# Optimization experiments

Measured on AMD Instinct MI355X. Metric: run time of the kernel, lower is better.

## Reference

```python
import jax, jax.numpy as jnp
import numpy as np

B, S, E = 2, 2048, 2048
H = 16              # num value heads
D = E // H // 2     # = 64, half head dim (Q/K head dim)
LAMBDA_INIT = 0.8 - 0.6 * float(np.exp(-0.3 * 12))
NORM_EPS = 1e-5


def setup_inputs() -> dict:
    key = jax.random.key(0)
    ks = jax.random.split(key, 10)
    std = 0.02
    x = jax.random.normal(ks[0], (B, S, E), jnp.float32)
    Wq = jax.random.normal(ks[1], (E, E), jnp.float32) * std
    Wk = jax.random.normal(ks[2], (E, E), jnp.float32) * std
    Wv = jax.random.normal(ks[3], (E, E), jnp.float32) * std
    Wo = jax.random.normal(ks[4], (E, E), jnp.float32) * std
    lambda_q1 = jax.random.normal(ks[5], (D,), jnp.float32) * 0.1
    lambda_q2 = jax.random.normal(ks[6], (D,), jnp.float32) * 0.1
    lambda_k1 = jax.random.normal(ks[7], (D,), jnp.float32) * 0.1
    lambda_k2 = jax.random.normal(ks[8], (D,), jnp.float32) * 0.1
    norm_w = jnp.ones((2 * D,), jnp.float32)
    # standard RoPE angle table: (S, D//2)
    inv_freq = 1.0 / (10000.0 ** (np.arange(0, D, 2, dtype=np.float32) / D))
    ang = np.outer(np.arange(S, dtype=np.float32), inv_freq)
    freqs_cos = jnp.asarray(np.cos(ang), jnp.float32)
    freqs_sin = jnp.asarray(np.sin(ang), jnp.float32)
    return {"x": x, "Wq": Wq, "Wk": Wk, "Wv": Wv, "Wo": Wo,
            "lambda_q1": lambda_q1, "lambda_q2": lambda_q2,
            "lambda_k1": lambda_k1, "lambda_k2": lambda_k2,
            "norm_w": norm_w, "freqs_cos": freqs_cos, "freqs_sin": freqs_sin,
            "start_pos": 0}


def _rope(t, cos, sin):
    # t: (B, S, nh, D); complex rotation over pairs along last dim
    tr = t.reshape(*t.shape[:-1], -1, 2)
    tre, tim = tr[..., 0], tr[..., 1]
    c = cos[None, :, None, :]
    s = sin[None, :, None, :]
    out_re = tre * c - tim * s
    out_im = tre * s + tim * c
    return jnp.stack([out_re, out_im], axis=-1).reshape(t.shape)


def reference(x, Wq, Wk, Wv, Wo, lambda_q1, lambda_q2, lambda_k1, lambda_k2,
              norm_w, freqs_cos, freqs_sin, start_pos):
    bsz, tgt_len, _ = x.shape
    scaling = D ** (-0.5)
    q = (x @ Wq.T).reshape(bsz, tgt_len, 2 * H, D)
    k = (x @ Wk.T).reshape(bsz, tgt_len, 2 * H, D)
    v = (x @ Wv.T).reshape(bsz, tgt_len, H, 2 * D)
    q = _rope(q, freqs_cos, freqs_sin)
    k = _rope(k, freqs_cos, freqs_sin)
    q = (q * scaling).transpose(0, 2, 1, 3)      # (B, 2H, S, D)
    keys = k.transpose(0, 2, 1, 3)               # (B, 2H, S, D)
    values = v.transpose(0, 2, 1, 3)             # (B, H, S, 2D)
    scores = jnp.einsum('bhsd,bhtd->bhst', q, keys)
    causal = jnp.where(jnp.arange(tgt_len)[None, :] > jnp.arange(tgt_len)[:, None],
                       jnp.float32(-jnp.inf), jnp.float32(0.0))
    scores = scores + causal
    attn = jax.nn.softmax(scores.astype(jnp.float32), axis=-1)
    lam1 = jnp.exp(jnp.sum(lambda_q1 * lambda_k1))
    lam2 = jnp.exp(jnp.sum(lambda_q2 * lambda_k2))
    lambda_full = lam1 - lam2 + LAMBDA_INIT
    attn = attn.reshape(bsz, H, 2, tgt_len, tgt_len)
    attn_diff = attn[:, :, 0] - lambda_full * attn[:, :, 1]   # (B, H, S, S)
    ctx = jnp.einsum('bhst,bhtd->bhsd', attn_diff, values)    # (B, H, S, 2D)
    # per-head RMSNorm over 2D channel dim
    ctx = ctx * jax.lax.rsqrt(jnp.mean(ctx * ctx, axis=-1, keepdims=True) + NORM_EPS)
    ctx = ctx * norm_w
    ctx = ctx.transpose(0, 2, 1, 3).reshape(bsz, tgt_len, H * 2 * D)
    return ctx @ Wo.T
```

## Files before the change

### kernel.cpp

```cpp
#include <hip/hip_runtime.h>
#include <hip/hip_bf16.h>
#include <stdint.h>

typedef __hip_bfloat16 bf16;
typedef __attribute__((ext_vector_type(8))) short short8;
typedef __attribute__((ext_vector_type(4))) short s4v;
typedef __attribute__((ext_vector_type(4))) float floatx4;

#define MFMA16(a, b, c) __builtin_amdgcn_mfma_f32_16x16x32_bf16((a), (b), (c), 0, 0, 0)
#define LAMBDA_INIT_F 0.7836057665f

__device__ __forceinline__ void async16(const void* g, void* l) {
    __builtin_amdgcn_global_load_lds(
        (const __attribute__((address_space(1))) void*)g,
        (__attribute__((address_space(3))) void*)(uintptr_t)l,
        16, 0, 0);
}

__device__ __forceinline__ float loadf(const void* p, size_t idx, int isbf) {
    if (isbf) return __bfloat162float(((const bf16*)p)[idx]);
    return ((const float*)p)[idx];
}

__global__ void detect_dtype(const unsigned short* __restrict__ x, int* __restrict__ flag) {
    const int t = threadIdx.x;
    const unsigned short u = x[2 * t];
    const int e = (u >> 7) & 0xFF;
    int sane = (e >= 110 && e <= 130) ? 1 : 0;
#pragma unroll
    for (int m = 32; m > 0; m >>= 1) sane += __shfl_xor(sane, m);
    if (t == 0) flag[0] = (sane >= 32) ? 1 : 0;
}

__global__ __launch_bounds__(256) void to_bf16(const void* __restrict__ src,
                                               bf16* __restrict__ dst, int n,
                                               const int* __restrict__ flag,
                                               int skip_if_bf16) {
    if (skip_if_bf16 && flag[0]) return;
    const int i = (blockIdx.x * 256 + threadIdx.x) * 8;
    if (i >= n) return;
    if (flag[0]) {
        *(short8*)(dst + i) = *(const short8*)((const bf16*)src + i);
    } else {
        const float* f = (const float*)src + i;
        short8 r;
#pragma unroll
        for (int j = 0; j < 8; ++j) {
            bf16 h = __float2bfloat16(f[j]);
            r[j] = __builtin_bit_cast(short, h);
        }
        *(short8*)(dst + i) = r;
    }
}

__device__ __forceinline__ void gemm_core(const bf16* __restrict__ A,
                                          const bf16* __restrict__ B,
                                          void* __restrict__ C,
                                          int N, int K, int bm, int bn,
                                          const int* __restrict__ flag,
                                          const void* __restrict__ fcos,
                                          const void* __restrict__ fsin,
                                          int mode, bf16* As, bf16* Bs) {
    const int tid  = threadIdx.x;
    const int lane = tid & 63;
    const int quad = lane >> 4;
    const int l16  = lane & 15;
    const int w    = tid >> 6;
    const int wr   = w >> 1, wc = w & 1;

    floatx4 acc[4][4];
#pragma unroll
    for (int i = 0; i < 4; ++i)
#pragma unroll
        for (int j = 0; j < 4; ++j)
#pragma unroll
            for (int r = 0; r < 4; ++r) acc[i][j][r] = 0.0f;

    for (int k0 = 0; k0 < K; k0 += 32) {
        __syncthreads();
#pragma unroll
        for (int i = 0; i < 2; ++i) {
            const int c     = i * 256 + tid;
            const int row   = c >> 2;
            const int inner = c & 3;
            async16(A + (size_t)(bm * 128 + row) * K + k0 + inner * 8, (char*)As + c * 16);
            async16(B + (size_t)(bn * 128 + row) * K + k0 + inner * 8, (char*)Bs + c * 16);
        }
        __syncthreads();

        short8 af[4], bfr[4];
#pragma unroll
        for (int i = 0; i < 4; ++i)
            af[i] = *(const short8*)((const char*)As + (wr * 64 + i * 16 + l16) * 64 + quad * 16);
#pragma unroll
        for (int j = 0; j < 4; ++j)
            bfr[j] = *(const short8*)((const char*)Bs + (wc * 64 + j * 16 + l16) * 64 + quad * 16);
#pragma unroll
        for (int i = 0; i < 4; ++i)
#pragma unroll
            for (int j = 0; j < 4; ++j)
                acc[i][j] = MFMA16(af[i], bfr[j], acc[i][j]);
    }

    const int isbf = flag[0];
    if (mode == 3) {
#pragma unroll
        for (int i = 0; i < 4; ++i)
#pragma unroll
            for (int j = 0; j < 4; ++j) {
                const int n  = bn * 128 + wc * 64 + j * 16 + l16;
                const int m0 = bm * 128 + wr * 64 + i * 16 + quad * 4;
                const int bb = m0 >> 11;
                const int s0 = m0 & 2047;
                s4v pk;
#pragma unroll
                for (int r = 0; r < 4; ++r) {
                    bf16 hv = __float2bfloat16(acc[i][j][r]);
                    pk[r] = __builtin_bit_cast(short, hv);
                }
                *(s4v*)((bf16*)C + ((size_t)(bb * 2048 + n)) * 2048 + s0) = pk;
            }
    } else if (mode == 1 || mode == 2) {
        const float qs = (mode == 1) ? 0.125f : 1.0f;
#pragma unroll
        for (int i = 0; i < 4; ++i)
#pragma unroll
            for (int j = 0; j < 4; ++j) {
                const int n   = bn * 128 + wc * 64 + j * 16 + l16;
                const int jp  = (n & 63) >> 1;
                const float sg = (n & 1) ? 1.0f : -1.0f;
#pragma unroll
                for (int r = 0; r < 4; ++r) {
                    const int m = bm * 128 + wr * 64 + i * 16 + quad * 4 + r;
                    const int s = m & 2047;
                    const float v  = acc[i][j][r];
                    const float pv = __shfl_xor(v, 1);
                    const float ct = loadf(fcos, (size_t)s * 32 + jp, isbf);
                    const float st = loadf(fsin, (size_t)s * 32 + jp, isbf);
                    const float out = (v * ct + sg * pv * st) * qs;
                    ((bf16*)C)[(size_t)m * N + n] = __float2bfloat16(out);
                }
            }
    } else {
        const int c_bf = (mode == 4) ? isbf : 1;
#pragma unroll
        for (int i = 0; i < 4; ++i)
#pragma unroll
            for (int j = 0; j < 4; ++j) {
                const int n = bn * 128 + wc * 64 + j * 16 + l16;
#pragma unroll
                for (int r = 0; r < 4; ++r) {
                    const int m = bm * 128 + wr * 64 + i * 16 + quad * 4 + r;
                    if (c_bf) ((bf16*)C)[(size_t)m * N + n] = __float2bfloat16(acc[i][j][r]);
                    else      ((float*)C)[(size_t)m * N + n] = acc[i][j][r];
                }
            }
    }
}

__global__ __launch_bounds__(256) void gemm_bt_ep(const bf16* __restrict__ A,
                                                  const bf16* __restrict__ B,
                                                  void* __restrict__ C,
                                                  int M, int N, int K,
                                                  const int* __restrict__ flag,
                                                  const void* __restrict__ fcos,
                                                  const void* __restrict__ fsin,
                                                  int mode) {
    __shared__ __align__(16) bf16 As[128 * 32];
    __shared__ __align__(16) bf16 Bs[128 * 32];
    gemm_core(A, B, C, N, K, blockIdx.y, blockIdx.x, flag, fcos, fsin, mode, As, Bs);
}

__global__ __launch_bounds__(256) void gemm_qkv(const bf16* __restrict__ A,
                                                const bf16* __restrict__ Wq_s,
                                                const bf16* __restrict__ Wk_s,
                                                const bf16* __restrict__ Wv_s,
                                                const void* __restrict__ WqR,
                                                const void* __restrict__ WkR,
                                                const void* __restrict__ WvR,
                                                bf16* __restrict__ qbuf,
                                                bf16* __restrict__ kbuf,
                                                bf16* __restrict__ vtbuf,
                                                int K, const int* __restrict__ flag,
                                                const void* __restrict__ fcos,
                                                const void* __restrict__ fsin) {
    __shared__ __align__(16) bf16 As[128 * 32];
    __shared__ __align__(16) bf16 Bs[128 * 32];
    const int wsel = blockIdx.x >> 4;
    const int bnl  = blockIdx.x & 15;
    const int isbf = flag[0];
    const bf16* Bp;
    void* Cp;
    int mode;
    if (wsel == 0)      { Bp = isbf ? (const bf16*)WqR : Wq_s; Cp = qbuf;  mode = 1; }
    else if (wsel == 1) { Bp = isbf ? (const bf16*)WkR : Wk_s; Cp = kbuf;  mode = 2; }
    else                { Bp = isbf ? (const bf16*)WvR : Wv_s; Cp = vtbuf; mode = 3; }
    gemm_core(A, Bp, Cp, 2048, K, blockIdx.y, bnl, flag, fcos, fsin, mode, As, Bs);
}

__global__ void lambda_kernel(const void* lq1, const void* lq2,
                              const void* lk1, const void* lk2,
                              float* out, const int* __restrict__ flag) {
    const int isbf = flag[0];
    const int t = threadIdx.x;
    float p1 = loadf(lq1, t, isbf) * loadf(lk1, t, isbf);
    float p2 = loadf(lq2, t, isbf) * loadf(lk2, t, isbf);
#pragma unroll
    for (int m = 32; m > 0; m >>= 1) {
        p1 += __shfl_xor(p1, m);
        p2 += __shfl_xor(p2, m);
    }
    if (t == 0) out[0] = expf(p1) - expf(p2) + LAMBDA_INIT_F;
}

__global__ __launch_bounds__(256) void diff_attn(const bf16* __restrict__ Q,
                                                 const bf16* __restrict__ K,
                                                 const bf16* __restrict__ Vt,
                                                 bf16* __restrict__ ctx,
                                                 const float* __restrict__ lam,
                                                 const void* __restrict__ norm_w,
                                                 const int* __restrict__ flag) {
    __shared__ __align__(16) char smem[55296];
    bf16* K1s = (bf16*)smem;
    bf16* K2s = (bf16*)(smem + 8192);
    bf16* Vs  = (bf16*)(smem + 16384);
    char* pool = smem + 32768;

    const int isbf = flag[0];
    const int tid  = threadIdx.x;
    const int lane = tid & 63;
    const int quad = lane >> 4;
    const int l16  = lane & 15;
    const int w    = tid >> 6;
    const int t7   = l16 & 7;

    const int bidx = blockIdx.x;
    const int c8   = bidx & 7;
    const int r6   = bidx >> 3;
    const int p    = r6 & 15;
    const int grp  = (r6 >> 4) * 8 + c8;
    const int h    = grp & 15;
    const int b    = grp >> 4;

    const float lambda_full = lam[0];
    float nw[8];
#pragma unroll
    for (int j = 0; j < 8; ++j) nw[j] = loadf(norm_w, j * 16 + l16, isbf);

    bf16* P1s = (bf16*)(pool + w * 2816);
    bf16* P2s = (bf16*)(pool + 11264 + w * 2816);

    for (int tsel = 0; tsel < 2; ++tsel) {
        const int qt = tsel ? (31 - p) : p;
        const int q0 = qt * 64;

        __syncthreads();

#pragma unroll
        for (int i = 0; i < 2; ++i) {
            const int c = i * 256 + tid;
            const int row = c >> 3, cc = c & 7;
            const int inner = cc ^ (row & 7);
            async16(Q + ((size_t)(b * 2048 + q0 + row) * 32 + 2 * h) * 64 + inner * 8,
                    pool + c * 16);
            async16(Q + ((size_t)(b * 2048 + q0 + row) * 32 + 2 * h + 1) * 64 + inner * 8,
                    pool + 8192 + c * 16);
        }
        __syncthreads();

        short8 qf1[2], qf2[2];
        {
            const int rho = w * 16 + l16;
#pragma unroll
            for (int c = 0; c < 2; ++c) {
                const int ch = (c * 4 + quad) ^ t7;
                qf1[c] = *(const short8*)(pool + rho * 128 + ch * 16);
                qf2[c] = *(const short8*)(pool + 8192 + rho * 128 + ch * 16);
            }
        }

        floatx4 O1[8], O2[8];
#pragma unroll
        for (int j = 0; j < 8; ++j)
#pragma unroll
            for (int r = 0; r < 4; ++r) { O1[j][r] = 0.0f; O2[j][r] = 0.0f; }
        float lp1[4] = {0.f, 0.f, 0.f, 0.f};
        float lp2[4] = {0.f, 0.f, 0.f, 0.f};

        for (int kt0 = 0; kt0 <= q0; kt0 += 64) {
            __syncthreads();
#pragma unroll
            for (int i = 0; i < 2; ++i) {
                const int c = i * 256 + tid;
                const int row = c >> 3, cc = c & 7;
                const int inner = cc ^ (row & 7);
                async16(K + ((size_t)(b * 2048 + kt0 + row) * 32 + 2 * h) * 64 + inner * 8,
                        (char*)K1s + c * 16);
                async16(K + ((size_t)(b * 2048 + kt0 + row) * 32 + 2 * h + 1) * 64 + inner * 8,
                        (char*)K2s + c * 16);
            }
#pragma unroll
            for (int i = 0; i < 4; ++i) {
                const int c = i * 256 + tid;
                const int d = c >> 3, cc = c & 7;
                const int inner = cc ^ (d & 7);
                async16(Vt + ((size_t)(b * 16 + h) * 128 + d) * 2048 + kt0 + inner * 8,
                        (char*)Vs + c * 16);
            }
            __syncthreads();

            floatx4 s1[4], s2[4];
#pragma unroll
            for (int j = 0; j < 4; ++j)
#pragma unroll
                for (int r = 0; r < 4; ++r) { s1[j][r] = 0.0f; s2[j][r] = 0.0f; }
#pragma unroll
            for (int c = 0; c < 2; ++c) {
                const int ch = ((c * 4 + quad) ^ t7) * 16;
#pragma unroll
                for (int j = 0; j < 4; ++j) {
                    short8 k1f = *(const short8*)((const char*)K1s + (j * 16 + l16) * 128 + ch);
                    s1[j] = MFMA16(qf1[c], k1f, s1[j]);
                    short8 k2f = *(const short8*)((const char*)K2s + (j * 16 + l16) * 128 + ch);
                    s2[j] = MFMA16(qf2[c], k2f, s2[j]);
                }
            }

            if (kt0 == q0) {
#pragma unroll
                for (int j = 0; j < 4; ++j)
#pragma unroll
                    for (int r = 0; r < 4; ++r)
                        if (j * 16 + l16 > w * 16 + quad * 4 + r) {
                            s1[j][r] = -1e30f;
                            s2[j][r] = -1e30f;
                        }
            }

#pragma unroll
            for (int j = 0; j < 4; ++j)
#pragma unroll
                for (int r = 0; r < 4; ++r) {
                    const float e1 = __expf(s1[j][r]);
                    const float e2 = __expf(s2[j][r]);
                    lp1[r] += e1;
                    lp2[r] += e2;
                    P1s[(quad * 4 + r) * 88 + j * 16 + l16] = __float2bfloat16(e1);
                    P2s[(quad * 4 + r) * 88 + j * 16 + l16] = __float2bfloat16(e2);
                }

#pragma unroll
            for (int c = 0; c < 2; ++c) {
                short8 a1 = *(const short8*)((const char*)P1s + l16 * 176 + c * 64 + quad * 16);
                short8 a2 = *(const short8*)((const char*)P2s + l16 * 176 + c * 64 + quad * 16);
                const int ch = ((c * 4 + quad) ^ t7) * 16;
#pragma unroll
                for (int j = 0; j < 8; ++j) {
                    short8 vb = *(const short8*)((const char*)Vs + (j * 16 + l16) * 128 + ch);
                    O1[j] = MFMA16(a1, vb, O1[j]);
                    O2[j] = MFMA16(a2, vb, O2[j]);
                }
            }
        }

#pragma unroll
        for (int r = 0; r < 4; ++r) {
            float t1 = lp1[r], t2 = lp2[r];
            t1 += __shfl_xor(t1, 1); t2 += __shfl_xor(t2, 1);
            t1 += __shfl_xor(t1, 2); t2 += __shfl_xor(t2, 2);
            t1 += __shfl_xor(t1, 4); t2 += __shfl_xor(t2, 4);
            t1 += __shfl_xor(t1, 8); t2 += __shfl_xor(t2, 8);
            const float i1 = 1.0f / t1;
            const float i2 = lambda_full / t2;
            float cv[8];
            float ss = 0.0f;
#pragma unroll
            for (int j = 0; j < 8; ++j) {
                const float v = O1[j][r] * i1 - O2[j][r] * i2;
                cv[j] = v;
                ss += v * v;
            }
            ss += __shfl_xor(ss, 1);
            ss += __shfl_xor(ss, 2);
            ss += __shfl_xor(ss, 4);
            ss += __shfl_xor(ss, 8);
            const float scale = rsqrtf(ss * (1.0f / 128.0f) + 1e-5f);
            const int row = q0 + w * 16 + quad * 4 + r;
            const size_t base = ((size_t)(b * 2048) + row) * 2048 + h * 128;
#pragma unroll
            for (int j = 0; j < 8; ++j)
                ctx[base + j * 16 + l16] = __float2bfloat16(cv[j] * scale * nw[j]);
        }
    }
}

extern "C" void kernel_launch(void* const* d_in, const int* in_sizes, int n_in,
                              void* d_out, int out_size, void* d_ws, size_t ws_size,
                              hipStream_t stream) {
    const void* x   = d_in[0];
    const void* Wq  = d_in[1];
    const void* Wk  = d_in[2];
    const void* Wv  = d_in[3];
    const void* Wo  = d_in[4];
    const void* lq1 = d_in[5];
    const void* lq2 = d_in[6];
    const void* lk1 = d_in[7];
    const void* lk2 = d_in[8];
    const void* nw  = d_in[9];
    const void* fc  = d_in[10];
    const void* fs  = d_in[11];

    const size_t BUF = (size_t)4096 * 2048 * sizeof(bf16);
    if (ws_size < 4 * BUF + 64) return;
    char* ws = (char*)d_ws;
    bf16*  qbuf  = (bf16*)(ws);
    bf16*  kbuf  = (bf16*)(ws + BUF);
    bf16*  vbuf  = (bf16*)(ws + 2 * BUF);
    bf16*  vtbuf = (bf16*)(ws + 3 * BUF);
    float* lamb  = (float*)(ws + 4 * BUF);
    int*   flag  = (int*)(ws + 4 * BUF + 8);
    bf16*  xb    = vbuf;
    bf16*  ctxb  = vbuf;

    bf16* wq_s = (bf16*)d_out;
    bf16* wk_s = wq_s + (size_t)2048 * 2048;
    bf16* wv_s = wk_s + (size_t)2048 * 2048;

    const int NX = 2 * 2048 * 2048;
    const int NW = 2048 * 2048;

    detect_dtype<<<1, 64, 0, stream>>>((const unsigned short*)x, flag);
    to_bf16<<<NX / 2048, 256, 0, stream>>>(x, xb, NX, flag, 0);

    to_bf16<<<NW / 2048, 256, 0, stream>>>(Wq, wq_s, NW, flag, 1);
    to_bf16<<<NW / 2048, 256, 0, stream>>>(Wk, wk_s, NW, flag, 1);
    to_bf16<<<NW / 2048, 256, 0, stream>>>(Wv, wv_s, NW, flag, 1);

    dim3 gq(48, 32);
    gemm_qkv<<<gq, 256, 0, stream>>>(xb, wq_s, wk_s, wv_s, Wq, Wk, Wv,
                                     qbuf, kbuf, vtbuf, 2048, flag, fc, fs);

    lambda_kernel<<<1, 64, 0, stream>>>(lq1, lq2, lk1, lk2, lamb, flag);

    diff_attn<<<512, 256, 0, stream>>>(qbuf, kbuf, vtbuf, ctxb, lamb, nw, flag);

    to_bf16<<<NW / 2048, 256, 0, stream>>>(Wo, qbuf, NW, flag, 0);
    dim3 gg(16, 32);
    gemm_bt_ep<<<gg, 256, 0, stream>>>(ctxb, qbuf, d_out, 4096, 2048, 2048, flag, fc, fs, 4);
}
```

Baseline: 501.2 us.

## Rewrite GEMMs as 256x256 tiles with 4-stage async LDS pipeline and swizzle

Replaces the 128x128, single-buffered GEMM core with a 256x256 tile kernel using 512 threads and a 4-slot LDS ring filled by async global-to-LDS loads two steps ahead. Loads are split around two MFMA half-phases, with XOR swizzling to reduce LDS bank conflicts and s_setprio to favour MFMA issue. The aim is to hide global load latency and raise arithmetic intensity for the QKV and output projections. In exchange it uses 128KB of dynamic LDS per block and launches far fewer blocks (384 and 128), so the GPU may be underfilled or tail-limited.

```diff
diff --git a/kernel.cpp b/kernel.cpp
--- a/kernel.cpp
+++ b/kernel.cpp
@@ -53,69 +53,126 @@
     }
 }
 
-__device__ __forceinline__ void gemm_core(const bf16* __restrict__ A,
-                                          const bf16* __restrict__ B,
-                                          void* __restrict__ C,
-                                          int N, int K, int bm, int bn,
-                                          const int* __restrict__ flag,
-                                          const void* __restrict__ fcos,
-                                          const void* __restrict__ fsin,
-                                          int mode, bf16* As, bf16* Bs) {
+__device__ __forceinline__ void gemm256_core(const bf16* __restrict__ A,
+                                             const bf16* __restrict__ B,
+                                             void* __restrict__ C,
+                                             int N, int bm, int bnl,
+                                             const int* __restrict__ flag,
+                                             const void* __restrict__ fcos,
+                                             const void* __restrict__ fsin,
+                                             int mode, char* lds) {
+    const int K = 2048;
+    const int NT = K / 32;
+
     const int tid  = threadIdx.x;
     const int lane = tid & 63;
     const int quad = lane >> 4;
     const int l16  = lane & 15;
     const int w    = tid >> 6;
-    const int wr   = w >> 1, wc = w & 1;
-
-    floatx4 acc[4][4];
-#pragma unroll
-    for (int i = 0; i < 4; ++i)
-#pragma unroll
-        for (int j = 0; j < 4; ++j)
-#pragma unroll
-            for (int r = 0; r < 4; ++r) acc[i][j][r] = 0.0f;
-
-    for (int k0 = 0; k0 < K; k0 += 32) {
-        __syncthreads();
-#pragma unroll
-        for (int i = 0; i < 2; ++i) {
-            const int c     = i * 256 + tid;
-            const int row   = c >> 2;
-            const int inner = c & 3;
-            async16(A + (size_t)(bm * 128 + row) * K + k0 + inner * 8, (char*)As + c * 16);
-            async16(B + (size_t)(bn * 128 + row) * K + k0 + inner * 8, (char*)Bs + c * 16);
-        }
-        __syncthreads();
-
-        short8 af[4], bfr[4];
-#pragma unroll
-        for (int i = 0; i < 4; ++i)
-            af[i] = *(const short8*)((const char*)As + (wr * 64 + i * 16 + l16) * 64 + quad * 16);
-#pragma unroll
-        for (int j = 0; j < 4; ++j)
-            bfr[j] = *(const short8*)((const char*)Bs + (wc * 64 + j * 16 + l16) * 64 + quad * 16);
-#pragma unroll
-        for (int i = 0; i < 4; ++i)
-#pragma unroll
-            for (int j = 0; j < 4; ++j)
-                acc[i][j] = MFMA16(af[i], bfr[j], acc[i][j]);
+    const int wr   = w >> 2;
+    const int wc   = w & 3;
+
+    const int c0 = tid, c1 = tid + 512;
+    const int r0 = c0 >> 2, r1 = c1 >> 2;
+    const int kc0 = (c0 & 3) ^ (((r0 >> 3) & 1) << 1);
+    const int kc1 = (c1 & 3) ^ (((r1 >> 3) & 1) << 1);
+    const bf16* Asrc0 = A + (size_t)(bm * 256 + r0) * K + kc0 * 8;
+    const bf16* Asrc1 = A + (size_t)(bm * 256 + r1) * K + kc1 * 8;
+    const bf16* Bsrc0 = B + (size_t)(bnl * 256 + r0) * K + kc0 * 8;
+    const bf16* Bsrc1 = B + (size_t)(bnl * 256 + r1) * K + kc1 * 8;
+    const int dA0 = c0 * 16, dA1 = c1 * 16;
+    const int dB0 = 16384 + c0 * 16, dB1 = 16384 + c1 * 16;
+
+    const int swz = (quad * 16) ^ ((l16 & 8) << 2);
+    int offA[8], offB[4];
+#pragma unroll
+    for (int f = 0; f < 8; ++f) offA[f] = (wr * 128 + f * 16 + l16) * 64 + swz;
+#pragma unroll
+    for (int g = 0; g < 4; ++g) offB[g] = 16384 + (wc * 64 + g * 16 + l16) * 64 + swz;
+
+    floatx4 acc[8][4];
+#pragma unroll
+    for (int f = 0; f < 8; ++f)
+#pragma unroll
+        for (int g = 0; g < 4; ++g)
+#pragma unroll
+            for (int r = 0; r < 4; ++r) acc[f][g][r] = 0.0f;
+
+#pragma unroll
+    for (int ts = 0; ts < 2; ++ts) {
+        char* slot = lds + ts * 32768;
+        async16(Asrc0 + ts * 32, slot + dA0);
+        async16(Asrc1 + ts * 32, slot + dA1);
+        async16(Bsrc0 + ts * 32, slot + dB0);
+        async16(Bsrc1 + ts * 32, slot + dB1);
     }
-
-    const int isbf = flag[0];
+    asm volatile("s_waitcnt vmcnt(4)" ::: "memory");
+    __builtin_amdgcn_s_barrier();
+    asm volatile("" ::: "memory");
+
+#pragma unroll 4
+    for (int t = 0; t < NT; ++t) {
+        char* slot  = lds + (t & 3) * 32768;
+        const int ts = t + 2;
+        char* wslot = lds + (ts & 3) * 32768;
+
+        short8 af[4], bfv[4];
+#pragma unroll
+        for (int f = 0; f < 4; ++f) af[f] = *(const short8*)(slot + offA[f]);
+#pragma unroll
+        for (int g = 0; g < 4; ++g) bfv[g] = *(const short8*)(slot + offB[g]);
+        if (ts < NT) {
+            async16(Asrc0 + (size_t)ts * 32, wslot + dA0);
+            async16(Asrc1 + (size_t)ts * 32, wslot + dA1);
+        }
+        asm volatile("" ::: "memory");
+        __builtin_amdgcn_s_barrier();
+        asm volatile("" ::: "memory");
+        __builtin_amdgcn_s_setprio(1);
+#pragma unroll
+        for (int f = 0; f < 4; ++f)
+#pragma unroll
+            for (int g = 0; g < 4; ++g)
+                acc[f][g] = MFMA16(af[f], bfv[g], acc[f][g]);
+        __builtin_amdgcn_s_setprio(0);
+
+        short8 af2[4];
+#pragma unroll
+        for (int f = 0; f < 4; ++f) af2[f] = *(const short8*)(slot + offA[4 + f]);
+        if (ts < NT) {
+            async16(Bsrc0 + (size_t)ts * 32, wslot + dB0);
+            async16(Bsrc1 + (size_t)ts * 32, wslot + dB1);
+            asm volatile("s_waitcnt vmcnt(4)" ::: "memory");
+        } else {
+            asm volatile("s_waitcnt vmcnt(0)" ::: "memory");
+        }
+        __builtin_amdgcn_s_barrier();
+        asm volatile("" ::: "memory");
+        __builtin_amdgcn_s_setprio(1);
+#pragma unroll
+        for (int f = 0; f < 4; ++f)
+#pragma unroll
+            for (int g = 0; g < 4; ++g)
+                acc[4 + f][g] = MFMA16(af2[f], bfv[g], acc[4 + f][g]);
+        __builtin_amdgcn_s_setprio(0);
+    }
+
+    const int isbf  = flag[0];
+    const int mbase = bm * 256 + wr * 128;
+    const int nbase = bnl * 256 + wc * 64;
     if (mode == 3) {
 #pragma unroll
-        for (int i = 0; i < 4; ++i)
-#pragma unroll
-            for (int j = 0; j < 4; ++j) {
-                const int n  = bn * 128 + wc * 64 + j * 16 + l16;
-                const int m0 = bm * 128 + wr * 64 + i * 16 + quad * 4;
+        for (int f = 0; f < 8; ++f)
+#pragma unroll
+            for (int g = 0; g < 4; ++g) {
+                const int n  = nbase + g * 16 + l16;
+                const int m0 = mbase + f * 16 + quad * 4;
                 const int bb = m0 >> 11;
                 const int s0 = m0 & 2047;
                 s4v pk;
 #pragma unroll
                 for (int r = 0; r < 4; ++r) {
-                    bf16 hv = __float2bfloat16(acc[i][j][r]);
+                    bf16 hv = __float2bfloat16(acc[f][g][r]);
                     pk[r] = __builtin_bit_cast(short, hv);
                 }
                 *(s4v*)((bf16*)C + ((size_t)(bb * 2048 + n)) * 2048 + s0) = pk;
@@ -123,17 +180,17 @@
     } else if (mode == 1 || mode == 2) {
         const float qs = (mode == 1) ? 0.125f : 1.0f;
 #pragma unroll
-        for (int i = 0; i < 4; ++i)
-#pragma unroll
-            for (int j = 0; j < 4; ++j) {
-                const int n   = bn * 128 + wc * 64 + j * 16 + l16;
+        for (int f = 0; f < 8; ++f)
+#pragma unroll
+            for (int g = 0; g < 4; ++g) {
+                const int n   = nbase + g * 16 + l16;
                 const int jp  = (n & 63) >> 1;
                 const float sg = (n & 1) ? 1.0f : -1.0f;
 #pragma unroll
                 for (int r = 0; r < 4; ++r) {
-                    const int m = bm * 128 + wr * 64 + i * 16 + quad * 4 + r;
+                    const int m = mbase + f * 16 + quad * 4 + r;
                     const int s = m & 2047;
-                    const float v  = acc[i][j][r];
+                    const float v  = acc[f][g][r];
                     const float pv = __shfl_xor(v, 1);
                     const float ct = loadf(fcos, (size_t)s * 32 + jp, isbf);
                     const float st = loadf(fsin, (size_t)s * 32 + jp, isbf);
@@ -144,50 +201,36 @@
     } else {
         const int c_bf = (mode == 4) ? isbf : 1;
 #pragma unroll
-        for (int i = 0; i < 4; ++i)
-#pragma unroll
-            for (int j = 0; j < 4; ++j) {
-                const int n = bn * 128 + wc * 64 + j * 16 + l16;
+        for (int f = 0; f < 8; ++f)
+#pragma unroll
+            for (int g = 0; g < 4; ++g) {
+                const int n = nbase + g * 16 + l16;
 #pragma unroll
                 for (int r = 0; r < 4; ++r) {
-                    const int m = bm * 128 + wr * 64 + i * 16 + quad * 4 + r;
-                    if (c_bf) ((bf16*)C)[(size_t)m * N + n] = __float2bfloat16(acc[i][j][r]);
-                    else      ((float*)C)[(size_t)m * N + n] = acc[i][j][r];
+                    const int m = mbase + f * 16 + quad * 4 + r;
+                    if (c_bf) ((bf16*)C)[(size_t)m * N + n] = __float2bfloat16(acc[f][g][r]);
+                    else      ((float*)C)[(size_t)m * N + n] = acc[f][g][r];
                 }
             }
     }
 }
 
-__global__ __launch_bounds__(256) void gemm_bt_ep(const bf16* __restrict__ A,
-                                                  const bf16* __restrict__ B,
-                                                  void* __restrict__ C,
-                                                  int M, int N, int K,
-                                                  const int* __restrict__ flag,
-                                                  const void* __restrict__ fcos,
-                                                  const void* __restrict__ fsin,
-                                                  int mode) {
-    __shared__ __align__(16) bf16 As[128 * 32];
-    __shared__ __align__(16) bf16 Bs[128 * 32];
-    gemm_core(A, B, C, N, K, blockIdx.y, blockIdx.x, flag, fcos, fsin, mode, As, Bs);
-}
-
-__global__ __launch_bounds__(256) void gemm_qkv(const bf16* __restrict__ A,
-                                                const bf16* __restrict__ Wq_s,
-                                                const bf16* __restrict__ Wk_s,
-                                                const bf16* __restrict__ Wv_s,
-                                                const void* __restrict__ WqR,
-                                                const void* __restrict__ WkR,
-                                                const void* __restrict__ WvR,
-                                                bf16* __restrict__ qbuf,
-                                                bf16* __restrict__ kbuf,
-                                                bf16* __restrict__ vtbuf,
-                                                int K, const int* __restrict__ flag,
-                                                const void* __restrict__ fcos,
-                                                const void* __restrict__ fsin) {
-    __shared__ __align__(16) bf16 As[128 * 32];
-    __shared__ __align__(16) bf16 Bs[128 * 32];
-    const int wsel = blockIdx.x >> 4;
-    const int bnl  = blockIdx.x & 15;
+__global__ __launch_bounds__(512, 2) void gemm256_qkv(const bf16* __restrict__ A,
+                                                      const bf16* __restrict__ Wq_s,
+                                                      const bf16* __restrict__ Wk_s,
+                                                      const bf16* __restrict__ Wv_s,
+                                                      const void* __restrict__ WqR,
+                                                      const void* __restrict__ WkR,
+                                                      const void* __restrict__ WvR,
+                                                      bf16* __restrict__ qbuf,
+                                                      bf16* __restrict__ kbuf,
+                                                      bf16* __restrict__ vtbuf,
+                                                      const int* __restrict__ flag,
+                                                      const void* __restrict__ fcos,
+                                                      const void* __restrict__ fsin) {
+    extern __shared__ char lds[];
+    const int wsel = blockIdx.x >> 3;
+    const int bnl  = blockIdx.x & 7;
     const int isbf = flag[0];
     const bf16* Bp;
     void* Cp;
@@ -195,7 +238,17 @@
     if (wsel == 0)      { Bp = isbf ? (const bf16*)WqR : Wq_s; Cp = qbuf;  mode = 1; }
     else if (wsel == 1) { Bp = isbf ? (const bf16*)WkR : Wk_s; Cp = kbuf;  mode = 2; }
     else                { Bp = isbf ? (const bf16*)WvR : Wv_s; Cp = vtbuf; mode = 3; }
-    gemm_core(A, Bp, Cp, 2048, K, blockIdx.y, bnl, flag, fcos, fsin, mode, As, Bs);
+    gemm256_core(A, Bp, Cp, 2048, blockIdx.y, bnl, flag, fcos, fsin, mode, lds);
+}
+
+__global__ __launch_bounds__(512, 2) void gemm256_ep(const bf16* __restrict__ A,
+                                                     const bf16* __restrict__ B,
+                                                     void* __restrict__ C,
+                                                     int N,
+                                                     const int* __restrict__ flag,
+                                                     int mode) {
+    extern __shared__ char lds[];
+    gemm256_core(A, B, C, N, blockIdx.y, blockIdx.x, flag, nullptr, nullptr, mode, lds);
 }
 
 __global__ void lambda_kernel(const void* lq1, const void* lq2,
@@ -429,6 +482,11 @@
     const int NX = 2 * 2048 * 2048;
     const int NW = 2048 * 2048;
 
+    hipFuncSetAttribute(reinterpret_cast<const void*>(gemm256_qkv),
+                        hipFuncAttributeMaxDynamicSharedMemorySize, 131072);
+    hipFuncSetAttribute(reinterpret_cast<const void*>(gemm256_ep),
+                        hipFuncAttributeMaxDynamicSharedMemorySize, 131072);
+
     detect_dtype<<<1, 64, 0, stream>>>((const unsigned short*)x, flag);
     to_bf16<<<NX / 2048, 256, 0, stream>>>(x, xb, NX, flag, 0);
 
@@ -436,15 +494,15 @@
     to_bf16<<<NW / 2048, 256, 0, stream>>>(Wk, wk_s, NW, flag, 1);
     to_bf16<<<NW / 2048, 256, 0, stream>>>(Wv, wv_s, NW, flag, 1);
 
-    dim3 gq(48, 32);
-    gemm_qkv<<<gq, 256, 0, stream>>>(xb, wq_s, wk_s, wv_s, Wq, Wk, Wv,
-                                     qbuf, kbuf, vtbuf, 2048, flag, fc, fs);
+    dim3 gq(24, 16);
+    gemm256_qkv<<<gq, 512, 131072, stream>>>(xb, wq_s, wk_s, wv_s, Wq, Wk, Wv,
+                                             qbuf, kbuf, vtbuf, flag, fc, fs);
 
     lambda_kernel<<<1, 64, 0, stream>>>(lq1, lq2, lk1, lk2, lamb, flag);
 
     diff_attn<<<512, 256, 0, stream>>>(qbuf, kbuf, vtbuf, ctxb, lamb, nw, flag);
 
     to_bf16<<<NW / 2048, 256, 0, stream>>>(Wo, qbuf, NW, flag, 0);
-    dim3 gg(16, 32);
-    gemm_bt_ep<<<gg, 256, 0, stream>>>(ctxb, qbuf, d_out, 4096, 2048, 2048, flag, fc, fs, 4);
-}
+    dim3 gf(8, 16);
+    gemm256_ep<<<gf, 512, 131072, stream>>>(ctxb, qbuf, d_out, 2048, flag, 4);
+}
```

New measurement: 489.5 us. -2.3%, faster.
